# Kernel optimization log

Measured on AMD Instinct MI355X. Metric: run time of the kernel, lower is better.

## Reference

```python
import jax, jax.numpy as jnp
import numpy as np

B, SEQ, HORIZON, NKEYS = 256, 512, 32, 8192
L1, HIDDEN, L2 = 64, 128, 64


def _lstm_layer(x, Wih, Whh, bih, bhh):
    # x: [B, T, IN]; PyTorch gate order i, f, g, o
    Bn, T, _ = x.shape
    H = Whh.shape[1]
    xT = jnp.transpose(x, (1, 0, 2))  # [T, B, IN]
    pre_x = jnp.einsum('tbi,gi->tbg', xT, Wih) + bih + bhh  # precompute input part

    def step(carry, px):
        h, c = carry
        gates = px + h @ Whh.T
        i, f, g, o = jnp.split(gates, 4, axis=-1)
        i = jax.nn.sigmoid(i); f = jax.nn.sigmoid(f)
        g = jnp.tanh(g); o = jax.nn.sigmoid(o)
        c = f * c + i * g
        h = o * jnp.tanh(c)
        return (h, c), h

    h0 = jnp.zeros((Bn, H), x.dtype)
    c0 = jnp.zeros((Bn, H), x.dtype)
    _, hs = jax.lax.scan(step, (h0, c0), pre_x)
    return jnp.transpose(hs, (1, 0, 2))  # [B, T, H]


def setup_inputs():
    key = jax.random.key(0)
    ks = jax.random.split(key, 20)
    s = 0.05
    inp = jax.random.normal(ks[0], (B, SEQ), jnp.float32)
    akey = jax.random.normal(ks[1], (NKEYS, SEQ), jnp.float32)
    aval = jax.random.normal(ks[2], (NKEYS, SEQ + HORIZON), jnp.float32)
    W1 = jax.random.normal(ks[3], (L1, HORIZON + 1), jnp.float32) * s
    b1 = jnp.zeros((L1,), jnp.float32)
    Wih0 = jax.random.normal(ks[4], (4 * HIDDEN, L1), jnp.float32) * s
    Whh0 = jax.random.normal(ks[5], (4 * HIDDEN, HIDDEN), jnp.float32) * s
    bih0 = jnp.zeros((4 * HIDDEN,), jnp.float32)
    bhh0 = jnp.zeros((4 * HIDDEN,), jnp.float32)
    Wih1 = jax.random.normal(ks[6], (4 * HIDDEN, HIDDEN), jnp.float32) * s
    Whh1 = jax.random.normal(ks[7], (4 * HIDDEN, HIDDEN), jnp.float32) * s
    bih1 = jnp.zeros((4 * HIDDEN,), jnp.float32)
    bhh1 = jnp.zeros((4 * HIDDEN,), jnp.float32)
    W2 = jax.random.normal(ks[8], (L2, HIDDEN), jnp.float32) * s
    b2 = jnp.zeros((L2,), jnp.float32)
    W3 = jax.random.normal(ks[9], (HORIZON, L2), jnp.float32) * s
    b3 = jnp.zeros((HORIZON,), jnp.float32)
    return {"input": inp, "attention_key": akey, "attention_value": aval,
            "W1": W1, "b1": b1,
            "Wih0": Wih0, "Whh0": Whh0, "bih0": bih0, "bhh0": bhh0,
            "Wih1": Wih1, "Whh1": Whh1, "bih1": bih1, "bhh1": bhh1,
            "W2": W2, "b2": b2, "W3": W3, "b3": b3}


def reference(input, attention_key, attention_value, W1, b1,
              Wih0, Whh0, bih0, bhh0, Wih1, Whh1, bih1, bhh1,
              W2, b2, W3, b3):
    Bn = input.shape[0]
    # masked distance softmax attention: zero out per-row argmax before softmax
    distance = input @ attention_key.T  # [B, NKEYS]
    max_idx = jnp.argmax(distance, axis=1)
    distance = distance.at[jnp.arange(Bn), max_idx].set(0.0)
    a = jax.nn.softmax(distance, axis=1)
    hist = a @ attention_value  # [B, SEQ + HORIZON]
    # vectorized sliding-window unfold: [B, SEQ, HORIZON]
    win = jnp.arange(SEQ)[:, None] + jnp.arange(HORIZON)[None, :]
    ref_feats = hist[:, win]
    x = jnp.concatenate([input[:, :, None], ref_feats], axis=2)  # [B, SEQ, HORIZON+1]
    x = jnp.tanh(x @ W1.T + b1)  # [B, SEQ, L1]
    h = _lstm_layer(x, Wih0, Whh0, bih0, bhh0)
    h = _lstm_layer(h, Wih1, Whh1, bih1, bhh1)
    h = jnp.tanh(h)
    last = h[:, -1, :]  # [B, HIDDEN]
    l2 = jnp.tanh(last @ W2.T + b2)
    return l2 @ W3.T + b3  # [B, HORIZON]
```

## Files before the change

kernel.cpp:

```cpp
#include <hip/hip_runtime.h>

typedef _Float16 h8 __attribute__((ext_vector_type(8)));
typedef _Float16 h4 __attribute__((ext_vector_type(4)));
typedef float f32x4 __attribute__((ext_vector_type(4)));

__device__ __forceinline__ float fsigm(float x) {
    return __builtin_amdgcn_rcpf(1.0f + __expf(-x));
}
__device__ __forceinline__ float ftanh(float x) {
    return 1.0f - 2.0f * __builtin_amdgcn_rcpf(1.0f + __expf(2.0f * x));
}
__device__ __forceinline__ float fexp2(float x) {
    return __builtin_amdgcn_exp2f(x);
}
__device__ __forceinline__ void lds_barrier() {
    asm volatile("s_waitcnt lgkmcnt(0)\n\ts_barrier" ::: "memory");
}

#define L2E  1.4426950408889634f
#define L2E2 2.8853900817779268f

__global__ __launch_bounds__(256) void k_distM(const float* __restrict__ A,
                                               const float* __restrict__ Bm,
                                               float* __restrict__ C) {
    __shared__ _Float16 Ah[64][40], Al[64][40];
    __shared__ _Float16 Bh[64][40], Bl[64][40];
    const int n0 = blockIdx.x * 64;
    const int m0 = blockIdx.y * 64;
    const int tid = threadIdx.x;
    const int lane = tid & 63, wv = tid >> 6;
    const int quad = lane >> 4, l15 = lane & 15;
    f32x4 acc[4];
#pragma unroll
    for (int i = 0; i < 4; ++i) acc[i] = (f32x4){0.f, 0.f, 0.f, 0.f};

    for (int kt = 0; kt < 512; kt += 32) {
        __syncthreads();
#pragma unroll
        for (int r = 0; r < 2; ++r) {
            int idx = tid + 256 * r;
            int m = idx >> 3, kq = (idx & 7) * 4;
            float4 v = *(const float4*)&A[(size_t)(m0 + m) * 512 + kt + kq];
            float e[4] = {v.x, v.y, v.z, v.w};
            h4 hi, lo;
#pragma unroll
            for (int j = 0; j < 4; ++j) {
                _Float16 h = (_Float16)e[j];
                hi[j] = h; lo[j] = (_Float16)(e[j] - (float)h);
            }
            *(h4*)&Ah[m][kq] = hi;
            *(h4*)&Al[m][kq] = lo;
        }
#pragma unroll
        for (int r = 0; r < 2; ++r) {
            int idx = tid + 256 * r;
            int n = idx >> 3, kq = (idx & 7) * 4;
            float4 v = *(const float4*)&Bm[(size_t)(n0 + n) * 512 + kt + kq];
            float e[4] = {v.x, v.y, v.z, v.w};
            h4 hi, lo;
#pragma unroll
            for (int j = 0; j < 4; ++j) {
                _Float16 h = (_Float16)e[j];
                hi[j] = h; lo[j] = (_Float16)(e[j] - (float)h);
            }
            *(h4*)&Bh[n][kq] = hi;
            *(h4*)&Bl[n][kq] = lo;
        }
        __syncthreads();
        h8 ah = *(const h8*)&Ah[wv * 16 + l15][quad * 8];
        h8 al = *(const h8*)&Al[wv * 16 + l15][quad * 8];
#pragma unroll
        for (int nt = 0; nt < 4; ++nt) {
            h8 bhf = *(const h8*)&Bh[nt * 16 + l15][quad * 8];
            h8 blf = *(const h8*)&Bl[nt * 16 + l15][quad * 8];
            acc[nt] = __builtin_amdgcn_mfma_f32_16x16x32_f16(ah, bhf, acc[nt], 0, 0, 0);
            acc[nt] = __builtin_amdgcn_mfma_f32_16x16x32_f16(al, bhf, acc[nt], 0, 0, 0);
            acc[nt] = __builtin_amdgcn_mfma_f32_16x16x32_f16(ah, blf, acc[nt], 0, 0, 0);
        }
    }
#pragma unroll
    for (int nt = 0; nt < 4; ++nt)
#pragma unroll
        for (int r = 0; r < 4; ++r)
            C[(size_t)(m0 + wv * 16 + quad * 4 + r) * 8192 + n0 + nt * 16 + l15] = acc[nt][r];
}

__global__ __launch_bounds__(512) void k_softmax(float* __restrict__ D) {
    __shared__ float row[8192];
    __shared__ float r1[512];
    __shared__ int   ri[512];
    __shared__ float r2[512];
    const int b = blockIdx.x, tid = threadIdx.x;
    float* dr = D + (size_t)b * 8192;
    for (int i = tid; i < 2048; i += 512)
        *(float4*)&row[i * 4] = *(const float4*)&dr[i * 4];
    __syncthreads();

    float m1 = -INFINITY, m2 = -INFINITY; int i1 = 0x7fffffff;
    for (int i = tid; i < 8192; i += 512) {
        float v = row[i];
        if (v > m1) { m2 = m1; m1 = v; i1 = i; }
        else        { m2 = fmaxf(m2, v); }
    }
    r1[tid] = m1; ri[tid] = i1; r2[tid] = m2;
    __syncthreads();
    for (int s = 256; s > 0; s >>= 1) {
        if (tid < s) {
            float am1 = r1[tid], bm1 = r1[tid + s];
            int   ai1 = ri[tid], bi1 = ri[tid + s];
            float am2 = r2[tid], bm2 = r2[tid + s];
            bool bwins = (bm1 > am1) || (bm1 == am1 && bi1 < ai1);
            float wm1 = bwins ? bm1 : am1;
            int   wi1 = bwins ? bi1 : ai1;
            float lm1 = bwins ? am1 : bm1;
            float wm2 = fmaxf(fmaxf(am2, bm2), lm1);
            r1[tid] = wm1; ri[tid] = wi1; r2[tid] = wm2;
        }
        __syncthreads();
    }
    const int   I1 = ri[0];
    const float M  = fmaxf(r2[0], 0.0f);
    __syncthreads();

    float ssum = 0.0f;
    for (int i = tid; i < 8192; i += 512) {
        float v = (i == I1) ? 0.0f : row[i];
        float e = __expf(v - M);
        row[i] = e;
        ssum += e;
    }
    r1[tid] = ssum;
    __syncthreads();
    for (int s = 256; s > 0; s >>= 1) {
        if (tid < s) r1[tid] += r1[tid + s];
        __syncthreads();
    }
    const float inv = 1.0f / r1[0];
    for (int i = tid; i < 2048; i += 512) {
        float4 v = *(float4*)&row[i * 4];
        v.x *= inv; v.y *= inv; v.z *= inv; v.w *= inv;
        *(float4*)&dr[i * 4] = v;
    }
}

__global__ __launch_bounds__(256) void k_histM(const float* __restrict__ A,
                                               const float* __restrict__ Bm,
                                               float* __restrict__ C) {
    __shared__ _Float16 Ah[64][40], Al[64][40];
    __shared__ _Float16 Bh[64][40], Bl[64][40];
    const int n0 = blockIdx.x * 64;
    const int m0 = blockIdx.y * 64;
    const int kz = blockIdx.z;
    const int tid = threadIdx.x;
    const int lane = tid & 63, wv = tid >> 6;
    const int quad = lane >> 4, l15 = lane & 15;
    const int bn = tid & 63;
    const int ko = (tid >> 6) * 8;
    const bool bok = (n0 + bn) < 544;
    f32x4 acc[4];
#pragma unroll
    for (int i = 0; i < 4; ++i) acc[i] = (f32x4){0.f, 0.f, 0.f, 0.f};

    const int k_lo = kz * 512, k_hi = k_lo + 512;
    for (int kt = k_lo; kt < k_hi; kt += 32) {
        __syncthreads();
#pragma unroll
        for (int r = 0; r < 2; ++r) {
            int idx = tid + 256 * r;
            int m = idx >> 3, kq = (idx & 7) * 4;
            float4 v = *(const float4*)&A[(size_t)(m0 + m) * 8192 + kt + kq];
            float e[4] = {v.x, v.y, v.z, v.w};
            h4 hi, lo;
#pragma unroll
            for (int j = 0; j < 4; ++j) {
                _Float16 h = (_Float16)e[j];
                hi[j] = h; lo[j] = (_Float16)(e[j] - (float)h);
            }
            *(h4*)&Ah[m][kq] = hi;
            *(h4*)&Al[m][kq] = lo;
        }
        {
            float e[8];
#pragma unroll
            for (int j = 0; j < 8; ++j)
                e[j] = bok ? Bm[(size_t)(kt + ko + j) * 544 + n0 + bn] : 0.f;
            h8 hi, lo;
#pragma unroll
            for (int j = 0; j < 8; ++j) {
                _Float16 h = (_Float16)e[j];
                hi[j] = h; lo[j] = (_Float16)(e[j] - (float)h);
            }
            *(h8*)&Bh[bn][ko] = hi;
            *(h8*)&Bl[bn][ko] = lo;
        }
        __syncthreads();
        h8 ah = *(const h8*)&Ah[wv * 16 + l15][quad * 8];
        h8 al = *(const h8*)&Al[wv * 16 + l15][quad * 8];
#pragma unroll
        for (int nt = 0; nt < 4; ++nt) {
            h8 bhf = *(const h8*)&Bh[nt * 16 + l15][quad * 8];
            h8 blf = *(const h8*)&Bl[nt * 16 + l15][quad * 8];
            acc[nt] = __builtin_amdgcn_mfma_f32_16x16x32_f16(ah, bhf, acc[nt], 0, 0, 0);
            acc[nt] = __builtin_amdgcn_mfma_f32_16x16x32_f16(al, bhf, acc[nt], 0, 0, 0);
            acc[nt] = __builtin_amdgcn_mfma_f32_16x16x32_f16(ah, blf, acc[nt], 0, 0, 0);
        }
    }
#pragma unroll
    for (int nt = 0; nt < 4; ++nt)
#pragma unroll
        for (int r = 0; r < 4; ++r) {
            int n = n0 + nt * 16 + l15;
            if (n < 544)
                atomicAdd(&C[(size_t)(m0 + wv * 16 + quad * 4 + r) * 544 + n], acc[nt][r]);
        }
}

__global__ __launch_bounds__(256) void k_xfeat(const float* __restrict__ inp,
                                               const float* __restrict__ hist,
                                               const float* __restrict__ W1,
                                               const float* __restrict__ b1,
                                               float* __restrict__ X) {
    __shared__ float w[33 * 64];
    __shared__ float bl[64];
    __shared__ float il[128];
    __shared__ float hl[160];
    const int t0 = blockIdx.x * 128;
    const int b  = blockIdx.y;
    const int tid = threadIdx.x;
    for (int idx = tid; idx < 2112; idx += 256) {
        int o = idx / 33, k = idx % 33;
        w[k * 64 + o] = W1[idx];
    }
    if (tid < 64) bl[tid] = b1[tid];
    if (tid < 128) il[tid] = inp[(size_t)b * 512 + t0 + tid];
    for (int i = tid; i < 159; i += 256) hl[i] = hist[(size_t)b * 544 + t0 + i];
    __syncthreads();
    const int o = tid & 63, tq = tid >> 6;
    for (int it = 0; it < 32; ++it) {
        int tl = it * 4 + tq;
        float acc = fmaf(il[tl], w[o], bl[o]);
#pragma unroll
        for (int j = 0; j < 32; ++j)
            acc = fmaf(hl[tl + j], w[(1 + j) * 64 + o], acc);
        X[(size_t)(b * 512 + t0 + tl) * 64 + o] = ftanh(acc);
    }
}

template <int K>
__device__ __forceinline__ void pregemm_mfma(const float* __restrict__ A,
                                             const float* __restrict__ Bw,
                                             const float* __restrict__ bih,
                                             const float* __restrict__ bhh,
                                             float* __restrict__ C,
                                             int t0, int tcs, int gb, float* sm) {
    _Float16* Ah = (_Float16*)sm;
    _Float16* Al = Ah + 128 * 40;
    _Float16* Bh = Al + 128 * 40;
    _Float16* Bl = Bh + 128 * 40;
    const int n0 = (gb & 3) * 128;
    const int m0 = (gb >> 2) * 128;
    const int tid = threadIdx.x;
    const int lane = tid & 63, wv = tid >> 6;
    const int quad = lane >> 4, l15 = lane & 15;
    const int tcm = (1 << tcs) - 1;
    const int lr0 = tid >> 3, lr1 = lr0 + 64;
    const int kq  = (tid & 7) * 4;
    const int gr0 = m0 + lr0, gr1 = m0 + lr1;
    const size_t ar0 = ((size_t)(gr0 >> tcs) * 512 + t0 + (gr0 & tcm)) * K;
    const size_t ar1 = ((size_t)(gr1 >> tcs) * 512 + t0 + (gr1 & tcm)) * K;
    const size_t br0 = (size_t)(n0 + lr0) * K;
    const size_t br1 = (size_t)(n0 + lr1) * K;
    const float sb0 = (((n0 + lr0) >> 7) == 2) ? L2E2 : L2E;
    const float sb1 = (((n0 + lr1) >> 7) == 2) ? L2E2 : L2E;

    f32x4 acc[8];
#pragma unroll
    for (int i = 0; i < 8; ++i) acc[i] = (f32x4){0.f, 0.f, 0.f, 0.f};

    float4 va0 = *(const float4*)&A[ar0 + kq];
    float4 va1 = *(const float4*)&A[ar1 + kq];
    float4 vb0 = *(const float4*)&Bw[br0 + kq];
    float4 vb1 = *(const float4*)&Bw[br1 + kq];

    for (int kt = 0; kt < K; kt += 32) {
        lds_barrier();
        {
            float e[4]; h4 hi, lo;
            e[0] = va0.x; e[1] = va0.y; e[2] = va0.z; e[3] = va0.w;
#pragma unroll
            for (int j = 0; j < 4; ++j) {
                _Float16 h = (_Float16)e[j];
                hi[j] = h; lo[j] = (_Float16)(e[j] - (float)h);
            }
            *(h4*)&Ah[lr0 * 40 + kq] = hi; *(h4*)&Al[lr0 * 40 + kq] = lo;
            e[0] = va1.x; e[1] = va1.y; e[2] = va1.z; e[3] = va1.w;
#pragma unroll
            for (int j = 0; j < 4; ++j) {
                _Float16 h = (_Float16)e[j];
                hi[j] = h; lo[j] = (_Float16)(e[j] - (float)h);
            }
            *(h4*)&Ah[lr1 * 40 + kq] = hi; *(h4*)&Al[lr1 * 40 + kq] = lo;
            e[0] = vb0.x * sb0; e[1] = vb0.y * sb0; e[2] = vb0.z * sb0; e[3] = vb0.w * sb0;
#pragma unroll
            for (int j = 0; j < 4; ++j) {
                _Float16 h = (_Float16)e[j];
                hi[j] = h; lo[j] = (_Float16)(e[j] - (float)h);
            }
            *(h4*)&Bh[lr0 * 40 + kq] = hi; *(h4*)&Bl[lr0 * 40 + kq] = lo;
            e[0] = vb1.x * sb1; e[1] = vb1.y * sb1; e[2] = vb1.z * sb1; e[3] = vb1.w * sb1;
#pragma unroll
            for (int j = 0; j < 4; ++j) {
                _Float16 h = (_Float16)e[j];
                hi[j] = h; lo[j] = (_Float16)(e[j] - (float)h);
            }
            *(h4*)&Bh[lr1 * 40 + kq] = hi; *(h4*)&Bl[lr1 * 40 + kq] = lo;
        }
        lds_barrier();
        if (kt + 32 < K) {
            va0 = *(const float4*)&A[ar0 + kt + 32 + kq];
            va1 = *(const float4*)&A[ar1 + kt + 32 + kq];
            vb0 = *(const float4*)&Bw[br0 + kt + 32 + kq];
            vb1 = *(const float4*)&Bw[br1 + kt + 32 + kq];
        }
        h8 ah = *(const h8*)&Ah[(wv * 16 + l15) * 40 + quad * 8];
        h8 al = *(const h8*)&Al[(wv * 16 + l15) * 40 + quad * 8];
#pragma unroll
        for (int nt = 0; nt < 8; ++nt) {
            h8 bhf = *(const h8*)&Bh[(nt * 16 + l15) * 40 + quad * 8];
            h8 blf = *(const h8*)&Bl[(nt * 16 + l15) * 40 + quad * 8];
            acc[nt] = __builtin_amdgcn_mfma_f32_16x16x32_f16(ah, bhf, acc[nt], 0, 0, 0);
            acc[nt] = __builtin_amdgcn_mfma_f32_16x16x32_f16(al, bhf, acc[nt], 0, 0, 0);
            acc[nt] = __builtin_amdgcn_mfma_f32_16x16x32_f16(ah, blf, acc[nt], 0, 0, 0);
        }
    }
#pragma unroll
    for (int nt = 0; nt < 8; ++nt) {
        const int n = n0 + nt * 16 + l15;
        const float sc = ((n >> 7) == 2) ? L2E2 : L2E;
        const float bb = (bih[n] + bhh[n]) * sc;
#pragma unroll
        for (int r = 0; r < 4; ++r)
            C[(size_t)(m0 + wv * 16 + quad * 4 + r) * 512 + n] = acc[nt][r] + bb;
    }
}

__device__ __forceinline__ _Float16* hpl(float* sm, int buf, int b) {
    return (_Float16*)sm + ((buf * 16 + b) * 136);
}

template <int RB>
__device__ __forceinline__ void rec_step(
        float* sm,
        const h8 (&wh)[4][4], const h8 (&wl)[4][4],
        f32x4 (&pc)[4],
        const float*& pp,
        float*& hob, bool wr, bool last,
        float (&c)[4],
        float* __restrict__ Sh, float* __restrict__ Sc,
        int l15, int quad, int un) {
    const _Float16* hp = hpl(sm, RB, l15);
    h8 hf[4];
#pragma unroll
    for (int q = 0; q < 4; ++q)
        hf[q] = *(const h8*)&hp[q * 32 + quad * 8];

    f32x4 aH[4], aL[4];
#pragma unroll
    for (int g = 0; g < 4; ++g) {
        aH[g] = pc[g];
        aL[g] = (f32x4){0.f, 0.f, 0.f, 0.f};
    }
#pragma unroll
    for (int g = 0; g < 4; ++g)
        pc[g] = *(const f32x4*)(pp + g * 128);
    pp += 512;

#pragma unroll
    for (int q = 0; q < 4; ++q) {
#pragma unroll
        for (int g = 0; g < 4; ++g) {
            aH[g] = __builtin_amdgcn_mfma_f32_16x16x32_f16(wh[g][q], hf[q], aH[g], 0, 0, 0);
            aL[g] = __builtin_amdgcn_mfma_f32_16x16x32_f16(wl[g][q], hf[q], aL[g], 0, 0, 0);
        }
    }

    f32x4 hv;
#pragma unroll
    for (int r = 0; r < 4; ++r) {
        float a0 = aH[0][r] + aL[0][r];
        float a1 = aH[1][r] + aL[1][r];
        float a2 = aH[2][r] + aL[2][r];
        float a3 = aH[3][r] + aL[3][r];
        float iv = __builtin_amdgcn_rcpf(1.0f + fexp2(-a0));
        float fv = __builtin_amdgcn_rcpf(1.0f + fexp2(-a1));
        float gv = 1.0f - 2.0f * __builtin_amdgcn_rcpf(1.0f + fexp2(a2));
        float ov = __builtin_amdgcn_rcpf(1.0f + fexp2(-a3));
        c[r] = fv * c[r] + iv * gv;
        float th = 1.0f - 2.0f * __builtin_amdgcn_rcpf(1.0f + fexp2(c[r] * L2E2));
        hv[r] = ov * th;
    }
    h4 hh;
#pragma unroll
    for (int j = 0; j < 4; ++j) hh[j] = (_Float16)hv[j];
    *(h4*)&hpl(sm, 1 - RB, l15)[un] = hh;
    if (wr) {
        __builtin_nontemporal_store(hv, (f32x4*)hob);
        hob += 128;
    }
    if (last) {
        *(f32x4*)Sh = hv;
        f32x4 cv = {c[0], c[1], c[2], c[3]};
        *(f32x4*)Sc = cv;
    }
    lds_barrier();
}

__device__ __forceinline__ void rec_body(const float* __restrict__ P,
                                         const float* __restrict__ Whh,
                                         float* __restrict__ S,
                                         float* __restrict__ Hout,
                                         int t0, int TC, int blk, float* sm) {
    const int b0   = blk * 16;
    const int tid  = threadIdx.x;
    const int lane = tid & 63;
    const int wv   = tid >> 6;
    const int quad = lane >> 4;
    const int l15  = lane & 15;
    const int un   = wv * 16 + quad * 4;
    const int nrow = wv * 16 + l15;

    h8 wh[4][4], wl[4][4];
    const float gs[4] = {L2E, L2E, L2E2, L2E};
#pragma unroll
    for (int g = 0; g < 4; ++g) {
        const float sc = gs[g];
        int n = g * 128 + nrow;
#pragma unroll
        for (int q = 0; q < 4; ++q) {
            int kb = q * 32 + quad * 8;
            const float* wp = &Whh[(size_t)n * 128 + kb];
            float4 w0 = *(const float4*)wp;
            float4 w1 = *(const float4*)(wp + 4);
            float we[8] = {w0.x, w0.y, w0.z, w0.w, w1.x, w1.y, w1.z, w1.w};
#pragma unroll
            for (int j = 0; j < 8; ++j) {
                float w = we[j] * sc;
                _Float16 hi = (_Float16)w;
                wh[g][q][j] = hi;
                wl[g][q][j] = (_Float16)(w - (float)hi);
            }
        }
    }

    float* Sh = S + (size_t)(b0 + l15) * 128 + un;
    float* Sc = Sh + 32768;
    float4 h0 = *(const float4*)Sh;
    float4 c0 = *(const float4*)Sc;
    float c[4] = {c0.x, c0.y, c0.z, c0.w};
    {
        h4 hh;
        hh[0] = (_Float16)h0.x; hh[1] = (_Float16)h0.y;
        hh[2] = (_Float16)h0.z; hh[3] = (_Float16)h0.w;
        *(h4*)&hpl(sm, 0, l15)[un] = hh;
    }

    const bool wr = (Hout != nullptr);
    float* hob = wr ? (Hout + ((size_t)(b0 + l15) * 512 + t0) * 128 + un) : nullptr;

    const float* pp = P + (size_t)(b0 + l15) * TC * 512 + un;
    f32x4 pcA[4], pcB[4];
#pragma unroll
    for (int g = 0; g < 4; ++g) pcA[g] = *(const f32x4*)(pp + g * 128);
#pragma unroll
    for (int g = 0; g < 4; ++g) pcB[g] = *(const f32x4*)(pp + 512 + g * 128);
    pp += 1024;

    lds_barrier();

    for (int tl = 0; tl < TC; tl += 2) {
        rec_step<0>(sm, wh, wl, pcA, pp, hob, wr, false, c, Sh, Sc, l15, quad, un);
        rec_step<1>(sm, wh, wl, pcB, pp, hob, wr, (tl + 2 == TC), c, Sh, Sc, l15, quad, un);
    }
}

__global__ __launch_bounds__(512, 1) void k_fused(
        const float* __restrict__ X,    const float* __restrict__ H0,
        const float* __restrict__ Wih0, const float* __restrict__ Wih1,
        const float* __restrict__ bih0, const float* __restrict__ bhh0,
        const float* __restrict__ bih1, const float* __restrict__ bhh1,
        const float* __restrict__ Whh0, const float* __restrict__ Whh1,
        const float* __restrict__ P0r, float* __restrict__ P0w,
        const float* __restrict__ P1r, float* __restrict__ P1w,
        float* __restrict__ S0, float* __restrict__ S1, float* __restrict__ H0out,
        int tr0, int tr1, int tp0, int tp1,
        int v_rec0, int v_rec1, int v_pre0, int v_pre1,
        int TC, int tcs) {
    __shared__ float smem[20480];
    const int bid = blockIdx.x;
    if (bid < 16) {
        if (v_rec0) rec_body(P0r, Whh0, S0, H0out, tr0, TC, bid, smem);
        return;
    }
    if (bid < 32) {
        if (v_rec1) rec_body(P1r, Whh1, S1, nullptr, tr1, TC, bid - 16, smem);
        return;
    }
    int gb = bid - 32;
    const int npre = 8 * TC;
    if (gb < npre) {
        if (v_pre0) pregemm_mfma<64>(X, Wih0, bih0, bhh0, P0w, tp0, tcs, gb, smem);
        return;
    }
    gb -= npre;
    if (v_pre1) pregemm_mfma<128>(H0, Wih1, bih1, bhh1, P1w, tp1, tcs, gb, smem);
}

__global__ __launch_bounds__(64) void k_tail(const float* __restrict__ Hs,
                                             const float* __restrict__ W2,
                                             const float* __restrict__ b2,
                                             const float* __restrict__ W3,
                                             const float* __restrict__ b3,
                                             float* __restrict__ out) {
    __shared__ float last[128], l2s[64];
    const int b = blockIdx.x, tid = threadIdx.x;
    last[tid]      = ftanh(Hs[(size_t)b * 128 + tid]);
    last[tid + 64] = ftanh(Hs[(size_t)b * 128 + 64 + tid]);
    __syncthreads();
    float acc = b2[tid];
#pragma unroll 4
    for (int j = 0; j < 128; ++j) acc = fmaf(W2[(size_t)tid * 128 + j], last[j], acc);
    l2s[tid] = ftanh(acc);
    __syncthreads();
    if (tid < 32) {
        float a2 = b3[tid];
#pragma unroll 4
        for (int o = 0; o < 64; ++o) a2 = fmaf(W3[(size_t)tid * 64 + o], l2s[o], a2);
        out[(size_t)b * 32 + tid] = a2;
    }
}

extern "C" void kernel_launch(void* const* d_in, const int* in_sizes, int n_in,
                              void* d_out, int out_size, void* d_ws, size_t ws_size,
                              hipStream_t stream) {
    (void)in_sizes; (void)n_in; (void)out_size;
    const float* inp  = (const float*)d_in[0];
    const float* akey = (const float*)d_in[1];
    const float* aval = (const float*)d_in[2];
    const float* W1   = (const float*)d_in[3];
    const float* b1   = (const float*)d_in[4];
    const float* Wih0 = (const float*)d_in[5];
    const float* Whh0 = (const float*)d_in[6];
    const float* bih0 = (const float*)d_in[7];
    const float* bhh0 = (const float*)d_in[8];
    const float* Wih1 = (const float*)d_in[9];
    const float* Whh1 = (const float*)d_in[10];
    const float* bih1 = (const float*)d_in[11];
    const float* bhh1 = (const float*)d_in[12];
    const float* W2   = (const float*)d_in[13];
    const float* b2   = (const float*)d_in[14];
    const float* W3   = (const float*)d_in[15];
    const float* b3   = (const float*)d_in[16];

    float* ws   = (float*)d_ws;
    float* dist = ws;
    float* hist = dist + 2097152;
    float* X    = hist + 139264;
    float* S0   = X + 8388672;
    float* S1   = S0 + 65536;
    float* H0   = S1 + 65536;
    float* PB   = H0 + 16777216;

    const int TC = 16, tcs = 4;
    const size_t pchunk = (size_t)256 * TC * 512 + 2048;
    float* P0b[2] = {PB, PB + pchunk};
    float* P1b[2] = {PB + 2 * pchunk, PB + 3 * pchunk};
    (void)ws_size;

    k_distM<<<dim3(128, 4), 256, 0, stream>>>(inp, akey, dist);
    k_softmax<<<256, 512, 0, stream>>>(dist);
    hipMemsetAsync(hist, 0, 139264 * 4, stream);
    k_histM<<<dim3(9, 4, 16), 256, 0, stream>>>(dist, aval, hist);
    k_xfeat<<<dim3(4, 256), 256, 0, stream>>>(inp, hist, W1, b1, X);
    hipMemsetAsync(S0, 0, (size_t)2 * 65536 * 4, stream);

    const int NC = 512 / TC;
    const int nblocks = 32 + 16 * TC;
    for (int k = -1; k <= NC + 1; ++k) {
        int v_rec0 = (k >= 0 && k < NC);
        int v_rec1 = (k >= 2 && k < NC + 2);
        int v_pre0 = (k + 1 >= 0 && k + 1 < NC);
        int v_pre1 = (k - 1 >= 0 && k - 1 < NC);
        if (!(v_rec0 | v_rec1 | v_pre0 | v_pre1)) continue;
        const float* P0r = P0b[k & 1];
        float*       P0w = P0b[(k + 1) & 1];
        const float* P1r = P1b[k & 1];
        float*       P1w = P1b[(k + 1) & 1];
        k_fused<<<nblocks, 512, 0, stream>>>(
            X, H0, Wih0, Wih1, bih0, bhh0, bih1, bhh1, Whh0, Whh1,
            P0r, P0w, P1r, P1w, S0, S1, H0,
            k * TC, (k - 2) * TC, (k + 1) * TC, (k - 1) * TC,
            v_rec0, v_rec1, v_pre0, v_pre1, TC, tcs);
    }
    k_tail<<<256, 64, 0, stream>>>(S1, W2, b2, W3, b3, (float*)d_out);
}
```

Before: 1.171 ms.

## Prefetch next k-tile in distance GEMM and enlarge LSTM time chunk when workspace allows

The distance GEMM kernel now loads the next k-tile of A and B into registers while the current tile's MFMAs run, and uses a lighter LDS-only barrier. Separately, the host doubles the LSTM time-chunk size (TC 16 to 32) when the workspace is large enough, which halves the number of chunked launches. The prefetch adds register pressure, and the larger chunk needs more workspace memory.

```diff
diff --git a/kernel.cpp b/kernel.cpp
--- a/kernel.cpp
+++ b/kernel.cpp
@@ -34,39 +34,52 @@
 #pragma unroll
     for (int i = 0; i < 4; ++i) acc[i] = (f32x4){0.f, 0.f, 0.f, 0.f};
 
+    int sm_[2], skq_[2];
+    size_t arow[2], brow[2];
+#pragma unroll
+    for (int r = 0; r < 2; ++r) {
+        int idx = tid + 256 * r;
+        sm_[r] = idx >> 3; skq_[r] = (idx & 7) * 4;
+        arow[r] = (size_t)(m0 + sm_[r]) * 512 + skq_[r];
+        brow[r] = (size_t)(n0 + sm_[r]) * 512 + skq_[r];
+    }
+    float4 va[2], vb[2];
+#pragma unroll
+    for (int r = 0; r < 2; ++r) {
+        va[r] = *(const float4*)&A[arow[r]];
+        vb[r] = *(const float4*)&Bm[brow[r]];
+    }
+
     for (int kt = 0; kt < 512; kt += 32) {
-        __syncthreads();
+        lds_barrier();
 #pragma unroll
         for (int r = 0; r < 2; ++r) {
-            int idx = tid + 256 * r;
-            int m = idx >> 3, kq = (idx & 7) * 4;
-            float4 v = *(const float4*)&A[(size_t)(m0 + m) * 512 + kt + kq];
-            float e[4] = {v.x, v.y, v.z, v.w};
+            float e[4] = {va[r].x, va[r].y, va[r].z, va[r].w};
             h4 hi, lo;
 #pragma unroll
             for (int j = 0; j < 4; ++j) {
                 _Float16 h = (_Float16)e[j];
                 hi[j] = h; lo[j] = (_Float16)(e[j] - (float)h);
             }
-            *(h4*)&Ah[m][kq] = hi;
-            *(h4*)&Al[m][kq] = lo;
-        }
-#pragma unroll
-        for (int r = 0; r < 2; ++r) {
-            int idx = tid + 256 * r;
-            int n = idx >> 3, kq = (idx & 7) * 4;
-            float4 v = *(const float4*)&Bm[(size_t)(n0 + n) * 512 + kt + kq];
-            float e[4] = {v.x, v.y, v.z, v.w};
-            h4 hi, lo;
+            *(h4*)&Ah[sm_[r]][skq_[r]] = hi;
+            *(h4*)&Al[sm_[r]][skq_[r]] = lo;
+            float f[4] = {vb[r].x, vb[r].y, vb[r].z, vb[r].w};
 #pragma unroll
             for (int j = 0; j < 4; ++j) {
-                _Float16 h = (_Float16)e[j];
-                hi[j] = h; lo[j] = (_Float16)(e[j] - (float)h);
-            }
-            *(h4*)&Bh[n][kq] = hi;
-            *(h4*)&Bl[n][kq] = lo;
-        }
-        __syncthreads();
+                _Float16 h = (_Float16)f[j];
+                hi[j] = h; lo[j] = (_Float16)(f[j] - (float)h);
+            }
+            *(h4*)&Bh[sm_[r]][skq_[r]] = hi;
+            *(h4*)&Bl[sm_[r]][skq_[r]] = lo;
+        }
+        lds_barrier();
+        if (kt + 32 < 512) {
+#pragma unroll
+            for (int r = 0; r < 2; ++r) {
+                va[r] = *(const float4*)&A[arow[r] + kt + 32];
+                vb[r] = *(const float4*)&Bm[brow[r] + kt + 32];
+            }
+        }
         h8 ah = *(const h8*)&Ah[wv * 16 + l15][quad * 8];
         h8 al = *(const h8*)&Al[wv * 16 + l15][quad * 8];
 #pragma unroll
@@ -569,12 +582,13 @@
     float* S1   = S0 + 65536;
     float* H0   = S1 + 65536;
     float* PB   = H0 + 16777216;
-
-    const int TC = 16, tcs = 4;
+    const size_t fixed = (size_t)(PB - ws);
+
+    int TC = 16, tcs = 4;
+    if ((fixed + 4ull * ((size_t)256 * 32 * 512 + 2048)) * 4 <= ws_size) { TC = 32; tcs = 5; }
     const size_t pchunk = (size_t)256 * TC * 512 + 2048;
     float* P0b[2] = {PB, PB + pchunk};
     float* P1b[2] = {PB + 2 * pchunk, PB + 3 * pchunk};
-    (void)ws_size;
 
     k_distM<<<dim3(128, 4), 256, 0, stream>>>(inp, akey, dist);
     k_softmax<<<256, 512, 0, stream>>>(dist);
```

New measurement: 1.003 ms. 1.17x faster.
